# Kernel optimization log

Hardware: AMD Instinct MI355X
Metric: run time of the kernel (lower is better)

## Reference

```python
import jax, jax.numpy as jnp
import numpy as np

B, S, E, H = 4, 2048, 1024, 16
D = E // H  # head_size = 64

def setup_inputs() -> dict:
    key = jax.random.key(0)
    k1, k2, k3 = jax.random.split(key, 3)
    x = jax.random.normal(k1, (B, S, E), dtype=jnp.float32)
    # torch Linear weight is (out,in); we store transposed (in,out) for x @ W
    w_attn = jax.random.normal(k2, (E, 3 * E), dtype=jnp.float32) * (1.0 / np.sqrt(E))
    w_proj = jax.random.normal(k3, (E, E), dtype=jnp.float32) * (1.0 / np.sqrt(E))
    return {"x": x, "w_attn": w_attn, "w_proj": w_proj}

def reference(x, w_attn, w_proj):
    b, s, e = x.shape
    qkv = x @ w_attn                      # (B,S,3E)
    q, k, v = jnp.split(qkv, 3, axis=2)
    # (B,S,H,D) -> (B,H,S,D)
    q = q.reshape(b, s, H, D).transpose(0, 2, 1, 3)
    k = k.reshape(b, s, H, D).transpose(0, 2, 1, 3)
    v = v.reshape(b, s, H, D).transpose(0, 2, 1, 3)
    scale = 1.0 / np.sqrt(D).astype(np.float32)
    att = jnp.einsum('bhqd,bhkd->bhqk', q, k) * scale  # (B,H,S,S)
    causal = jnp.tril(jnp.ones((s, s), dtype=bool))
    att = jnp.where(causal[None, None, :, :], att, jnp.float32(-jnp.inf))
    att = jax.nn.softmax(att, axis=-1)
    # dropout layers are identity in eval mode
    y = jnp.einsum('bhqk,bhkd->bhqd', att, v)          # (B,H,S,D)
    y = y.transpose(0, 2, 1, 3).reshape(b, s, e)       # (B,S,E)
    return y @ w_proj
```

## Files before the change

kernel.cpp:

```cpp
#include <hip/hip_runtime.h>
#include <hip/hip_bf16.h>
#include <cstdint>

typedef __attribute__((ext_vector_type(8))) short bf16x8;
typedef __attribute__((ext_vector_type(4))) short short4v;
typedef __attribute__((ext_vector_type(4))) float f32x4;

#define MFMA(a, b, c) __builtin_amdgcn_mfma_f32_16x16x32_bf16((a), (b), (c), 0, 0, 0)

__device__ __forceinline__ unsigned short f2bf(float f) {
  union { float f; unsigned int u; } v;
  v.f = f;
  unsigned int r = v.u + 0x7FFFu + ((v.u >> 16) & 1u);
  return (unsigned short)(r >> 16);
}

__device__ __forceinline__ unsigned int cvtpk(float lo, float hi) {
  unsigned int r;
  asm("v_cvt_pk_bf16_f32 %0, %1, %2" : "=v"(r) : "v"(lo), "v"(hi));
  return r;
}

__device__ __forceinline__ void async_cp16(const unsigned short* g, unsigned short* l) {
  __builtin_amdgcn_global_load_lds(
      (const __attribute__((address_space(1))) unsigned int*)g,
      (__attribute__((address_space(3))) unsigned int*)l, 16, 0, 0);
}

__global__ __launch_bounds__(256) void cvt_x(const float* __restrict__ in,
                                             unsigned short* __restrict__ out) {
  size_t i = ((size_t)blockIdx.x * 256 + threadIdx.x) * 8;
  float4 a = *(const float4*)(in + i);
  float4 b = *(const float4*)(in + i + 4);
  bf16x8 p;
  p[0] = (short)f2bf(a.x); p[1] = (short)f2bf(a.y);
  p[2] = (short)f2bf(a.z); p[3] = (short)f2bf(a.w);
  p[4] = (short)f2bf(b.x); p[5] = (short)f2bf(b.y);
  p[6] = (short)f2bf(b.z); p[7] = (short)f2bf(b.w);
  *(bf16x8*)(out + i) = p;
}

__global__ __launch_bounds__(256) void transpose_cvt(const float* __restrict__ in,
                                                     unsigned short* __restrict__ out,
                                                     int K, int N) {
  __shared__ float tile[64][65];
  int k0 = blockIdx.x * 64;
  int n0 = blockIdx.y * 64;
  int c = threadIdx.x & 63;
  int rb = threadIdx.x >> 6;
#pragma unroll
  for (int i = 0; i < 16; ++i) {
    int r = rb * 16 + i;
    tile[r][c] = in[(size_t)(k0 + r) * N + (n0 + c)];
  }
  __syncthreads();
#pragma unroll
  for (int i = 0; i < 16; ++i) {
    int r = rb * 16 + i;
    out[(size_t)(n0 + r) * K + (k0 + c)] = f2bf(tile[c][r]);
  }
}

__global__ __launch_bounds__(256) void gemm_qkv(const unsigned short* __restrict__ X,
                                                const unsigned short* __restrict__ WT,
                                                unsigned short* __restrict__ qb,
                                                unsigned short* __restrict__ kb,
                                                unsigned short* __restrict__ vt) {
  const int K = 1024;
  __shared__ unsigned short As[128 * 64];
  __shared__ unsigned short Bs[128 * 64];
  int t = threadIdx.x, lane = t & 63, w = t >> 6;
  int quad = lane >> 4, l15 = lane & 15;
  int sl7 = l15 & 7;
  int wm = (w >> 1) * 64, wn = (w & 1) * 64;
  int row0 = blockIdx.y * 128, col0 = blockIdx.x * 128;
  int srow = w * 8 + (lane >> 3);
  int schunk = (lane & 7) ^ (lane >> 3);
  const unsigned short* aSrc = X + (size_t)(row0 + srow) * K + schunk * 8;
  const unsigned short* bSrc = WT + (size_t)(col0 + srow) * K + schunk * 8;
  unsigned short* ldsA = &As[(w * 8) * 64];
  unsigned short* ldsB = &Bs[(w * 8) * 64];
  f32x4 zero4 = {0.f, 0.f, 0.f, 0.f};
  f32x4 acc[4][4];
#pragma unroll
  for (int i = 0; i < 4; ++i)
#pragma unroll
    for (int j = 0; j < 4; ++j) acc[i][j] = zero4;

  for (int k0 = 0; k0 < K; k0 += 64) {
    __syncthreads();
#pragma unroll
    for (int i = 0; i < 4; ++i)
      async_cp16(aSrc + (size_t)i * 32 * K + k0, ldsA + i * 32 * 64);
#pragma unroll
    for (int i = 0; i < 4; ++i)
      async_cp16(bSrc + (size_t)i * 32 * K + k0, ldsB + i * 32 * 64);
    __syncthreads();
#pragma unroll
    for (int h = 0; h < 2; ++h) {
      bf16x8 af[4], bfr[4];
#pragma unroll
      for (int mt = 0; mt < 4; ++mt)
        af[mt] = *(const bf16x8*)&As[(wm + mt * 16 + l15) * 64 +
                                     ((h * 4 + quad) ^ sl7) * 8];
#pragma unroll
      for (int nt = 0; nt < 4; ++nt)
        bfr[nt] = *(const bf16x8*)&Bs[(wn + nt * 16 + l15) * 64 +
                                      ((h * 4 + quad) ^ sl7) * 8];
#pragma unroll
      for (int mt = 0; mt < 4; ++mt)
#pragma unroll
        for (int nt = 0; nt < 4; ++nt)
          acc[mt][nt] = MFMA(af[mt], bfr[nt], acc[mt][nt]);
    }
  }

  const float qscale = 0.125f * 1.4426950408889634f;
#pragma unroll
  for (int mt = 0; mt < 4; ++mt) {
    int rix0 = row0 + wm + mt * 16 + quad * 4;
    int b = rix0 >> 11;
    int s0 = rix0 & 2047;
#pragma unroll
    for (int nt = 0; nt < 4; ++nt) {
      int c = col0 + wn + nt * 16 + l15;
      int which = c >> 10;
      int e = c & 1023;
      int h = e >> 6, d = e & 63;
      size_t bh = (size_t)b * 16 + h;
      if (which == 2) {
        short4v pv;
#pragma unroll
        for (int r = 0; r < 4; ++r) pv[r] = (short)f2bf(acc[mt][nt][r]);
        *(short4v*)(vt + (bh * 64 + d) * 2048 + s0) = pv;
      } else {
        unsigned short* dst = (which == 0) ? qb : kb;
        float sc = (which == 0) ? qscale : 1.0f;
#pragma unroll
        for (int r = 0; r < 4; ++r)
          dst[(bh * 2048 + (s0 + r)) * 64 + d] = f2bf(acc[mt][nt][r] * sc);
      }
    }
  }
}

__global__ __launch_bounds__(256, 2) void flash_attn(const unsigned short* __restrict__ qb,
                                                     const unsigned short* __restrict__ kb,
                                                     const unsigned short* __restrict__ vt,
                                                     unsigned short* __restrict__ yb) {
  __shared__ unsigned short Ks[2][64 * 64];
  int idx = blockIdx.x;
  int p = idx >> 6;
  int sub = idx & 63;
  int bh = (sub & 7) * 8 + (sub >> 3);
  int t = threadIdx.x, lane = t & 63, w = t >> 6;
  int quad = lane >> 4, l15 = lane & 15;
  f32x4 zero4 = {0.f, 0.f, 0.f, 0.f};
  bf16x8 ones;
#pragma unroll
  for (int i = 0; i < 8; ++i) ones[i] = (short)0x3F80;
  int b = bh >> 4, h = bh & 15;

  int srow_st = t >> 3;
  int swz_st = (srow_st & 3) | (((srow_st >> 3) & 1) << 2);
  int sslot = (t & 7) ^ swz_st;
  const unsigned short* kp0 =
      kb + ((size_t)bh * 2048 + srow_st) * 64 + sslot * 8;
  const unsigned short* Vb = vt + (size_t)bh * (64 * 2048);
  int fbase = (l15 >> 2) * 8 + (l15 & 3);
  int rslot0 = (quad ^ (l15 & 7)) * 8;
  int rslot1 = ((quad ^ 4) ^ (l15 & 7)) * 8;

  for (int seg = 0; seg < 2; ++seg) {
    int qt = seg ? p : (15 - p);
    int qrow0 = qt * 128 + w * 32;
    int ktmax = 2 * qt + 1;

    bf16x8 aq0[2], aq1[2];
#pragma unroll
    for (int s = 0; s < 2; ++s) {
      const unsigned short* Qp =
          qb + ((size_t)bh * 2048 + qrow0 + s * 16 + l15) * 64 + quad * 8;
      aq0[s] = *(const bf16x8*)Qp;
      aq1[s] = *(const bf16x8*)(Qp + 32);
    }
    f32x4 o[2][4], accl[2];
#pragma unroll
    for (int s = 0; s < 2; ++s) {
      accl[s] = zero4;
#pragma unroll
      for (int nt = 0; nt < 4; ++nt) o[s][nt] = zero4;
    }

    __syncthreads();
    async_cp16(kp0, &Ks[0][t * 8]);
    async_cp16(kp0 + 32 * 64, &Ks[0][2048 + t * 8]);
    int cur = 0;

    bf16x8 vA0[4], vA1[4], vB0[4], vB1[4];

#define LOADV(KB, v0, v1)                                                     \
  do {                                                                        \
    _Pragma("unroll") for (int nt = 0; nt < 4; ++nt) {                        \
      const unsigned short* Vp =                                              \
          Vb + (size_t)(nt * 16 + l15) * 2048 + (KB) + quad * 8;              \
      (v0)[nt] = *(const bf16x8*)Vp;                                          \
      (v1)[nt] = *(const bf16x8*)(Vp + 32);                                   \
    }                                                                         \
  } while (0)

#define COMPUTE(KB, v0, v1)                                                   \
  do {                                                                        \
    int kbase = (KB);                                                         \
    const unsigned short* Kc = &Ks[cur][0];                                   \
    bf16x8 kf0[4], kf1[4];                                                    \
    _Pragma("unroll") for (int nt = 0; nt < 4; ++nt) {                        \
      int row = fbase + (nt & 1) * 4 + (nt >> 1) * 32;                        \
      kf0[nt] = *(const bf16x8*)&Kc[row * 64 + rslot0];                       \
      kf1[nt] = *(const bf16x8*)&Kc[row * 64 + rslot1];                       \
    }                                                                         \
    _Pragma("unroll") for (int s = 0; s < 2; ++s) {                           \
      int rowb = qrow0 + s * 16;                                              \
      if (kbase <= rowb + 15) {                             \
        f32x4 pv4[4];                                                         \
        _Pragma("unroll") for (int nt = 0; nt < 4; ++nt) {                    \
          f32x4 z = zero4;                                                    \
          z = MFMA(kf0[nt], aq0[s], z);                                       \
          z = MFMA(kf1[nt], aq1[s], z);                                       \
          pv4[nt] = z;                                                        \
        }                                                                     \
        if (kbase + 63 > rowb) {                    \
          int qg = rowb + l15;                                                \
          _Pragma("unroll") for (int nt = 0; nt < 4; ++nt) {                  \
            int colb = kbase + quad * 8 + (nt & 1) * 4 + ((nt >> 1) << 5);    \
            _Pragma("unroll") for (int r = 0; r < 4; ++r)                     \
              if (colb + r > qg) pv4[nt][r] = -1e30f;                         \
          }                                                                   \
        }                                                                     \
        _Pragma("unroll") for (int nt = 0; nt < 4; ++nt)                      \
          _Pragma("unroll") for (int r = 0; r < 4; ++r)                       \
            pv4[nt][r] = __builtin_amdgcn_exp2f(pv4[nt][r]);                  \
        union { unsigned int u[4]; bf16x8 v; } A0, A1;                        \
        A0.u[0] = cvtpk(pv4[0][0], pv4[0][1]);                                \
        A0.u[1] = cvtpk(pv4[0][2], pv4[0][3]);                                \
        A0.u[2] = cvtpk(pv4[1][0], pv4[1][1]);                                \
        A0.u[3] = cvtpk(pv4[1][2], pv4[1][3]);                                \
        A1.u[0] = cvtpk(pv4[2][0], pv4[2][1]);                                \
        A1.u[1] = cvtpk(pv4[2][2], pv4[2][3]);                                \
        A1.u[2] = cvtpk(pv4[3][0], pv4[3][1]);                                \
        A1.u[3] = cvtpk(pv4[3][2], pv4[3][3]);                                \
        bf16x8 ap0 = A0.v, ap1 = A1.v;                                        \
        accl[s] = MFMA(ap0, ones, accl[s]);                                   \
        accl[s] = MFMA(ap1, ones, accl[s]);                                   \
        _Pragma("unroll") for (int nt = 0; nt < 4; ++nt) {                    \
          o[s][nt] = MFMA(ap0, (v0)[nt], o[s][nt]);                           \
          o[s][nt] = MFMA(ap1, (v1)[nt], o[s][nt]);                           \
        }                                                                     \
      }                                                                       \
    }                                                                         \
  } while (0)

#define ITER(KT, cv0, cv1, nv0, nv1)                                          \
  do {                                                                        \
    int kb0 = (KT) * 64;                                                      \
    __syncthreads();     \
    if ((KT) < ktmax) {                                                       \
      const unsigned short* nk = kp0 + (size_t)(kb0 + 64) * 64;               \
      async_cp16(nk, &Ks[cur ^ 1][t * 8]);                                    \
      async_cp16(nk + 32 * 64, &Ks[cur ^ 1][2048 + t * 8]);                   \
    }                                                                         \
    if ((KT) + 1 <= ktmax && kb0 + 64 <= qrow0 + 31) LOADV(kb0 + 64, nv0, nv1); \
    if (kb0 <= qrow0 + 31) COMPUTE(kb0, cv0, cv1);                            \
    cur ^= 1;                                                                 \
  } while (0)

    LOADV(0, vA0, vA1);
    for (int kt = 0; kt <= ktmax; kt += 2) {
      ITER(kt, vA0, vA1, vB0, vB1);
      if (kt + 1 > ktmax) break;
      ITER(kt + 1, vB0, vB1, vA0, vA1);
    }
#undef ITER
#undef COMPUTE
#undef LOADV

#pragma unroll
    for (int s = 0; s < 2; ++s) {
      float inv[4];
#pragma unroll
      for (int r = 0; r < 4; ++r) inv[r] = 1.0f / accl[s][r];
#pragma unroll
      for (int nt = 0; nt < 4; ++nt) {
        int e = h * 64 + nt * 16 + l15;
#pragma unroll
        for (int r = 0; r < 4; ++r) {
          int srow_g = qrow0 + s * 16 + quad * 4 + r;
          yb[((size_t)b * 2048 + srow_g) * 1024 + e] = f2bf(o[s][nt][r] * inv[r]);
        }
      }
    }
  }
}

__global__ __launch_bounds__(256) void gemm_proj(const unsigned short* __restrict__ Y,
                                                 const unsigned short* __restrict__ WT,
                                                 float* __restrict__ out) {
  const int K = 1024;
  __shared__ unsigned short As[128 * 64];
  __shared__ unsigned short Bs[128 * 64];
  int t = threadIdx.x, lane = t & 63, w = t >> 6;
  int quad = lane >> 4, l15 = lane & 15;
  int sl7 = l15 & 7;
  int wm = (w >> 1) * 64, wn = (w & 1) * 64;
  int row0 = blockIdx.y * 128, col0 = blockIdx.x * 128;
  int srow = w * 8 + (lane >> 3);
  int schunk = (lane & 7) ^ (lane >> 3);
  const unsigned short* aSrc = Y + (size_t)(row0 + srow) * K + schunk * 8;
  const unsigned short* bSrc = WT + (size_t)(col0 + srow) * K + schunk * 8;
  unsigned short* ldsA = &As[(w * 8) * 64];
  unsigned short* ldsB = &Bs[(w * 8) * 64];
  f32x4 zero4 = {0.f, 0.f, 0.f, 0.f};
  f32x4 acc[4][4];
#pragma unroll
  for (int i = 0; i < 4; ++i)
#pragma unroll
    for (int j = 0; j < 4; ++j) acc[i][j] = zero4;

  for (int k0 = 0; k0 < K; k0 += 64) {
    __syncthreads();
#pragma unroll
    for (int i = 0; i < 4; ++i)
      async_cp16(aSrc + (size_t)i * 32 * K + k0, ldsA + i * 32 * 64);
#pragma unroll
    for (int i = 0; i < 4; ++i)
      async_cp16(bSrc + (size_t)i * 32 * K + k0, ldsB + i * 32 * 64);
    __syncthreads();
#pragma unroll
    for (int h = 0; h < 2; ++h) {
      bf16x8 af[4], bfr[4];
#pragma unroll
      for (int mt = 0; mt < 4; ++mt)
        af[mt] = *(const bf16x8*)&As[(wm + mt * 16 + l15) * 64 +
                                     ((h * 4 + quad) ^ sl7) * 8];
#pragma unroll
      for (int nt = 0; nt < 4; ++nt)
        bfr[nt] = *(const bf16x8*)&Bs[(wn + nt * 16 + l15) * 64 +
                                      ((h * 4 + quad) ^ sl7) * 8];
#pragma unroll
      for (int mt = 0; mt < 4; ++mt)
#pragma unroll
        for (int nt = 0; nt < 4; ++nt)
          acc[mt][nt] = MFMA(af[mt], bfr[nt], acc[mt][nt]);
    }
  }

#pragma unroll
  for (int mt = 0; mt < 4; ++mt) {
    int rix0 = row0 + wm + mt * 16 + quad * 4;
#pragma unroll
    for (int nt = 0; nt < 4; ++nt) {
      int c = col0 + wn + nt * 16 + l15;
#pragma unroll
      for (int r = 0; r < 4; ++r)
        out[(size_t)(rix0 + r) * 1024 + c] = acc[mt][nt][r];
    }
  }
}

extern "C" void kernel_launch(void* const* d_in, const int* in_sizes, int n_in,
                              void* d_out, int out_size, void* d_ws, size_t ws_size,
                              hipStream_t stream) {
  const float* x = (const float*)d_in[0];
  const float* w_attn = (const float*)d_in[1];
  const float* w_proj = (const float*)d_in[2];
  float* out = (float*)d_out;
  char* ws = (char*)d_ws;
  unsigned short* wT  = (unsigned short*)(ws + 0);
  unsigned short* wpT = (unsigned short*)(ws + 6291456);
  unsigned short* qb  = (unsigned short*)(ws + 8388608);
  unsigned short* kb  = (unsigned short*)(ws + 25165824);
  unsigned short* vt  = (unsigned short*)(ws + 41943040);
  unsigned short* xyb = (unsigned short*)(ws + 58720256);

  cvt_x<<<4096, 256, 0, stream>>>(x, xyb);
  transpose_cvt<<<dim3(16, 48), 256, 0, stream>>>(w_attn, wT, 1024, 3072);
  transpose_cvt<<<dim3(16, 16), 256, 0, stream>>>(w_proj, wpT, 1024, 1024);
  gemm_qkv<<<dim3(24, 64), 256, 0, stream>>>(xyb, wT, qb, kb, vt);
  flash_attn<<<dim3(512), 256, 0, stream>>>(qb, kb, vt, xyb);
  gemm_proj<<<dim3(8, 64), 256, 0, stream>>>(xyb, wpT, out);
}
```

Before: 249.8 us.

## Rewrite QKV GEMM as 256x256 tile, 8-wave, double-buffered pipelined kernel

The QKV projection GEMM moves from 128x128 tiles with 4 waves and a single LDS buffer to 256x256 tiles with 8 waves and a double-buffered LDS pipeline. Global-to-LDS async copies for the next k-tiles are interleaved with MFMA phases, ordered by explicit barriers, waitcnt and setprio. The goal is to hide global load latency and raise operand reuse per LDS byte. In exchange it uses 128KB of LDS per block and has fragile hand-written synchronisation, and the launch grid drops to 384 blocks, which may not fill all CUs evenly.

```diff
diff --git a/kernel.cpp b/kernel.cpp
--- a/kernel.cpp
+++ b/kernel.cpp
@@ -61,87 +61,188 @@
   }
 }
 
-__global__ __launch_bounds__(256) void gemm_qkv(const unsigned short* __restrict__ X,
-                                                const unsigned short* __restrict__ WT,
-                                                unsigned short* __restrict__ qb,
-                                                unsigned short* __restrict__ kb,
-                                                unsigned short* __restrict__ vt) {
+__global__ __launch_bounds__(512, 2) void gemm_qkv(const unsigned short* __restrict__ X,
+                                                   const unsigned short* __restrict__ WT,
+                                                   unsigned short* __restrict__ qb,
+                                                   unsigned short* __restrict__ kb,
+                                                   unsigned short* __restrict__ vt) {
   const int K = 1024;
-  __shared__ unsigned short As[128 * 64];
-  __shared__ unsigned short Bs[128 * 64];
+  __shared__ unsigned short As[2][256 * 64];
+  __shared__ unsigned short Bs[2][256 * 64];
   int t = threadIdx.x, lane = t & 63, w = t >> 6;
   int quad = lane >> 4, l15 = lane & 15;
   int sl7 = l15 & 7;
-  int wm = (w >> 1) * 64, wn = (w & 1) * 64;
-  int row0 = blockIdx.y * 128, col0 = blockIdx.x * 128;
-  int srow = w * 8 + (lane >> 3);
-  int schunk = (lane & 7) ^ (lane >> 3);
+  int wm = (w >> 2) * 64;
+  int wn = (w & 3) * 32;
+  int row0 = blockIdx.y * 256, col0 = blockIdx.x * 256;
+
+  int srow = t >> 3;
+  int schunk = (t & 7) ^ (srow & 7);
   const unsigned short* aSrc = X + (size_t)(row0 + srow) * K + schunk * 8;
   const unsigned short* bSrc = WT + (size_t)(col0 + srow) * K + schunk * 8;
-  unsigned short* ldsA = &As[(w * 8) * 64];
-  unsigned short* ldsB = &Bs[(w * 8) * 64];
+
+  f32x4 acc[2][4][2][2];
   f32x4 zero4 = {0.f, 0.f, 0.f, 0.f};
-  f32x4 acc[4][4];
-#pragma unroll
-  for (int i = 0; i < 4; ++i)
-#pragma unroll
-    for (int j = 0; j < 4; ++j) acc[i][j] = zero4;
-
-  for (int k0 = 0; k0 < K; k0 += 64) {
-    __syncthreads();
-#pragma unroll
-    for (int i = 0; i < 4; ++i)
-      async_cp16(aSrc + (size_t)i * 32 * K + k0, ldsA + i * 32 * 64);
-#pragma unroll
-    for (int i = 0; i < 4; ++i)
-      async_cp16(bSrc + (size_t)i * 32 * K + k0, ldsB + i * 32 * 64);
-    __syncthreads();
-#pragma unroll
-    for (int h = 0; h < 2; ++h) {
-      bf16x8 af[4], bfr[4];
-#pragma unroll
-      for (int mt = 0; mt < 4; ++mt)
-        af[mt] = *(const bf16x8*)&As[(wm + mt * 16 + l15) * 64 +
-                                     ((h * 4 + quad) ^ sl7) * 8];
-#pragma unroll
-      for (int nt = 0; nt < 4; ++nt)
-        bfr[nt] = *(const bf16x8*)&Bs[(wn + nt * 16 + l15) * 64 +
-                                      ((h * 4 + quad) ^ sl7) * 8];
-#pragma unroll
-      for (int mt = 0; mt < 4; ++mt)
-#pragma unroll
-        for (int nt = 0; nt < 4; ++nt)
-          acc[mt][nt] = MFMA(af[mt], bfr[nt], acc[mt][nt]);
-    }
-  }
+#pragma unroll
+  for (int mh = 0; mh < 2; ++mh)
+#pragma unroll
+    for (int mf = 0; mf < 4; ++mf)
+#pragma unroll
+      for (int nh = 0; nh < 2; ++nh)
+#pragma unroll
+        for (int nf = 0; nf < 2; ++nf) acc[mh][mf][nh][nf] = zero4;
+
+#define STG(DST, H, SRC, KT)                                         \
+  do {                                                               \
+    const unsigned short* g_ = (SRC) + (size_t)(H)*128 * K + (KT)*64;\
+    unsigned short* d_ = (DST) + (H)*8192;                           \
+    async_cp16(g_, d_ + t * 8);                                      \
+    async_cp16(g_ + (size_t)64 * K, d_ + 4096 + t * 8);              \
+  } while (0)
+
+#define LDA(S, MH, MF, KS)                                           \
+  (*(const bf16x8*)&As[S][((MH)*128 + wm + (MF)*16 + l15) * 64 +     \
+                          ((((KS)*4 + quad) ^ sl7) * 8)])
+#define LDB(S, NH, NF, KS)                                           \
+  (*(const bf16x8*)&Bs[S][((NH)*128 + wn + (NF)*16 + l15) * 64 +     \
+                          ((((KS)*4 + quad) ^ sl7) * 8)])
+
+#define RD(S, MH, NH)                                                \
+  _Pragma("unroll") for (int mf = 0; mf < 4; ++mf) {                 \
+    a0_[mf] = LDA(S, MH, mf, 0);                                     \
+    a1_[mf] = LDA(S, MH, mf, 1);                                     \
+  }                                                                  \
+  _Pragma("unroll") for (int nf = 0; nf < 2; ++nf) {                 \
+    b0_[nf] = LDB(S, NH, nf, 0);                                     \
+    b1_[nf] = LDB(S, NH, nf, 1);                                     \
+  }
+
+#define MM(MH, NH)                                                   \
+  __builtin_amdgcn_s_setprio(1);                                     \
+  _Pragma("unroll") for (int mf = 0; mf < 4; ++mf)                   \
+  _Pragma("unroll") for (int nf = 0; nf < 2; ++nf) {                 \
+    acc[MH][mf][NH][nf] = MFMA(a0_[mf], b0_[nf], acc[MH][mf][NH][nf]); \
+    acc[MH][mf][NH][nf] = MFMA(a1_[mf], b1_[nf], acc[MH][mf][NH][nf]); \
+  }                                                                  \
+  __builtin_amdgcn_s_setprio(0);
+
+  STG(Bs[0], 0, bSrc, 0);
+  STG(As[0], 0, aSrc, 0);
+  STG(Bs[0], 1, bSrc, 0);
+  STG(As[0], 1, aSrc, 0);
+  STG(Bs[1], 0, bSrc, 1);
+  STG(As[1], 0, aSrc, 1);
+  asm volatile("s_waitcnt vmcnt(4)" ::: "memory");
+  __builtin_amdgcn_s_barrier();
+  __builtin_amdgcn_sched_barrier(0);
+
+  for (int it = 0; it < 8; ++it) {
+    int kt0 = 2 * it;
+    bool more = (it < 7);
+    bf16x8 a0_[4], a1_[4], b0_[2], b1_[2];
+    {
+      RD(0, 0, 0)
+      STG(Bs[1], 1, bSrc, kt0 + 1);
+      __builtin_amdgcn_s_barrier();
+      MM(0, 0)
+      __builtin_amdgcn_s_barrier();
+    }
+    {
+      RD(0, 1, 0)
+      STG(As[1], 1, aSrc, kt0 + 1);
+      __builtin_amdgcn_s_barrier();
+      MM(1, 0)
+      __builtin_amdgcn_s_barrier();
+    }
+    {
+      RD(0, 0, 1)
+      if (more) STG(Bs[0], 0, bSrc, kt0 + 2);
+      __builtin_amdgcn_s_barrier();
+      MM(0, 1)
+      __builtin_amdgcn_s_barrier();
+    }
+    {
+      RD(0, 1, 1)
+      if (more) {
+        STG(As[0], 0, aSrc, kt0 + 2);
+        asm volatile("s_waitcnt vmcnt(4)" ::: "memory");
+      } else {
+        asm volatile("s_waitcnt vmcnt(0)" ::: "memory");
+      }
+      __builtin_amdgcn_s_barrier();
+      MM(1, 1)
+      __builtin_amdgcn_s_barrier();
+      __builtin_amdgcn_sched_barrier(0);
+    }
+    {
+      RD(1, 0, 0)
+      if (more) STG(Bs[0], 1, bSrc, kt0 + 2);
+      __builtin_amdgcn_s_barrier();
+      MM(0, 0)
+      __builtin_amdgcn_s_barrier();
+    }
+    {
+      RD(1, 1, 0)
+      if (more) STG(As[0], 1, aSrc, kt0 + 2);
+      __builtin_amdgcn_s_barrier();
+      MM(1, 0)
+      __builtin_amdgcn_s_barrier();
+    }
+    {
+      RD(1, 0, 1)
+      if (more) STG(Bs[1], 0, bSrc, kt0 + 3);
+      __builtin_amdgcn_s_barrier();
+      MM(0, 1)
+      __builtin_amdgcn_s_barrier();
+    }
+    {
+      RD(1, 1, 1)
+      if (more) STG(As[1], 0, aSrc, kt0 + 3);
+      asm volatile("s_waitcnt vmcnt(4)" ::: "memory");
+      __builtin_amdgcn_s_barrier();
+      MM(1, 1)
+      __builtin_amdgcn_s_barrier();
+      __builtin_amdgcn_sched_barrier(0);
+    }
+  }
+#undef STG
+#undef LDA
+#undef LDB
+#undef RD
+#undef MM
 
   const float qscale = 0.125f * 1.4426950408889634f;
 #pragma unroll
-  for (int mt = 0; mt < 4; ++mt) {
-    int rix0 = row0 + wm + mt * 16 + quad * 4;
-    int b = rix0 >> 11;
-    int s0 = rix0 & 2047;
-#pragma unroll
-    for (int nt = 0; nt < 4; ++nt) {
-      int c = col0 + wn + nt * 16 + l15;
-      int which = c >> 10;
-      int e = c & 1023;
-      int h = e >> 6, d = e & 63;
-      size_t bh = (size_t)b * 16 + h;
-      if (which == 2) {
-        short4v pv;
-#pragma unroll
-        for (int r = 0; r < 4; ++r) pv[r] = (short)f2bf(acc[mt][nt][r]);
-        *(short4v*)(vt + (bh * 64 + d) * 2048 + s0) = pv;
-      } else {
-        unsigned short* dst = (which == 0) ? qb : kb;
-        float sc = (which == 0) ? qscale : 1.0f;
-#pragma unroll
-        for (int r = 0; r < 4; ++r)
-          dst[(bh * 2048 + (s0 + r)) * 64 + d] = f2bf(acc[mt][nt][r] * sc);
-      }
-    }
-  }
+  for (int mh = 0; mh < 2; ++mh)
+#pragma unroll
+    for (int mf = 0; mf < 4; ++mf) {
+      int rix0 = row0 + mh * 128 + wm + mf * 16 + quad * 4;
+      int b = rix0 >> 11;
+      int s0 = rix0 & 2047;
+#pragma unroll
+      for (int nh = 0; nh < 2; ++nh)
+#pragma unroll
+        for (int nf = 0; nf < 2; ++nf) {
+          int c = col0 + nh * 128 + wn + nf * 16 + l15;
+          int which = c >> 10;
+          int e = c & 1023;
+          int hh = e >> 6, d = e & 63;
+          size_t bh = (size_t)b * 16 + hh;
+          if (which == 2) {
+            short4v pv;
+#pragma unroll
+            for (int r = 0; r < 4; ++r)
+              pv[r] = (short)f2bf(acc[mh][mf][nh][nf][r]);
+            *(short4v*)(vt + (bh * 64 + d) * 2048 + s0) = pv;
+          } else {
+            unsigned short* dst = (which == 0) ? qb : kb;
+            float sc = (which == 0) ? qscale : 1.0f;
+#pragma unroll
+            for (int r = 0; r < 4; ++r)
+              dst[(bh * 2048 + (s0 + r)) * 64 + d] = f2bf(acc[mh][mf][nh][nf][r] * sc);
+          }
+        }
+    }
 }
 
 __global__ __launch_bounds__(256, 2) void flash_attn(const unsigned short* __restrict__ qb,
@@ -385,7 +486,7 @@
   cvt_x<<<4096, 256, 0, stream>>>(x, xyb);
   transpose_cvt<<<dim3(16, 48), 256, 0, stream>>>(w_attn, wT, 1024, 3072);
   transpose_cvt<<<dim3(16, 16), 256, 0, stream>>>(w_proj, wpT, 1024, 1024);
-  gemm_qkv<<<dim3(24, 64), 256, 0, stream>>>(xyb, wT, qb, kb, vt);
+  gemm_qkv<<<dim3(12, 32), 512, 0, stream>>>(xyb, wT, qb, kb, vt);
   flash_attn<<<dim3(512), 256, 0, stream>>>(qb, kb, vt, xyb);
   gemm_proj<<<dim3(8, 64), 256, 0, stream>>>(xyb, wpT, out);
 }
```

New measurement: 269.2 us. +7.7%, slower.
